# Kernel optimization log

Measured on AMD Instinct MI355X. Metric: run time of the kernel, lower is better.

Reference implementation:

```python
import jax, jax.numpy as jnp
import numpy as np

# ---- fixed config (Linear_mvm defaults, XBAR 64x64) ----
ROW = 64; COL = 64
BIT_SLICE = 2; BIT_STREAM = 1
W_BITS = 16; W_FRAC = 12          # weight_bit_frac = weight_bits//4*3
I_BITS = 16; I_FRAC = 12          # input_bit_frac  = input_bits//4*3
ADC_BIT = 8                       # log2(ROW) + bit_slice (bit_stream==1)
ACM_BITS = 16; ACM_FRAC = 12
BSN = W_BITS // BIT_SLICE         # 8 slices per weight, MSB-first columns
STN = I_BITS // BIT_STREAM        # 16 input bit-streams, LSB-first
IN_F = 1024; OUT_F = 1024; BATCH = 256


def _bit_slice_weight(w_nonneg):
    # w_nonneg: [out, in] nonnegative -> sliced crossbar matrix [in, out*BSN] (MSB->LSB per channel)
    w_int = jnp.clip(jnp.round(w_nonneg * (2.0 ** W_FRAC)), 0.0, 2.0 ** W_BITS - 1.0)
    shifts = (BIT_SLICE * (BSN - 1 - jnp.arange(BSN))).astype(jnp.float32)
    sl = jnp.floor(w_int[..., None] / (2.0 ** shifts)) % (2 ** BIT_SLICE)  # [out,in,BSN]
    o, i = w_nonneg.shape
    return sl.transpose(1, 0, 2).reshape(i, o * BSN)


def _input_bits(x):
    # two's-complement fixed point, LSB-first bit planes: [b, in, STN]
    x_int = jnp.clip(jnp.round(x * (2.0 ** I_FRAC)), -(2.0 ** (I_BITS - 1)), 2.0 ** (I_BITS - 1) - 1.0)
    x_u = jnp.where(x_int < 0, x_int + 2.0 ** I_BITS, x_int)
    return jnp.floor(x_u[..., None] / (2.0 ** jnp.arange(I_BITS, dtype=jnp.float32))) % 2.0


def _tile(mat, r, c):
    # pad to tile multiples and reshape to [xr, xc, r, c]
    pr = (-mat.shape[0]) % r; pc = (-mat.shape[1]) % c
    m = jnp.pad(mat, ((0, pr), (0, pc)))
    xr, xc = m.shape[0] // r, m.shape[1] // c
    return m.reshape(xr, r, xc, c).transpose(0, 2, 1, 3)


def _adc(a):
    # uniform ADC quantization of the analog column current to ADC_BIT bits
    full = float(ROW * (2 ** BIT_SLICE - 1))
    step = full / (2.0 ** ADC_BIT - 1.0)
    return jnp.clip(jnp.round(a / step) * step, 0.0, full)


def _mvm_one_sign(bits_tiled, xbars):
    # bits_tiled [b, xr, ROW, STN]; xbars [xr, xc, ROW, COL]
    sw_slice = 2.0 ** (BIT_SLICE * (BSN - 1 - jnp.arange(BSN, dtype=jnp.float32)))  # MSB..LSB
    sw_stream = 2.0 ** (BIT_STREAM * jnp.arange(STN, dtype=jnp.float32))
    sw_stream = sw_stream.at[-1].multiply(-1.0)  # two's-complement MSB stream

    def step(acc, si):
        bi, w = si                                   # bi [b,xr,ROW]
        analog = jnp.einsum('brk,rckj->brcj', bi, xbars)  # [b,xr,xc,COL]
        analog = _adc(analog)
        b, xr, xc, _ = analog.shape
        dig = analog.reshape(b, xr, xc, COL // BSN, BSN) @ sw_slice  # shift-add slices
        return acc + w * dig, None

    b = bits_tiled.shape[0]; xr, xc = xbars.shape[0], xbars.shape[1]
    acc0 = jnp.zeros((b, xr, xc, COL // BSN), jnp.float32)
    streams = jnp.moveaxis(bits_tiled, -1, 0)  # [STN, b, xr, ROW]
    acc, _ = jax.lax.scan(step, acc0, (streams, sw_stream))
    return acc.sum(axis=1).reshape(b, xc * (COL // BSN))  # sum row tiles, flatten channels


def _forward(x, weight, bias):
    pos = _bit_slice_weight(jnp.maximum(weight, 0.0))
    neg = _bit_slice_weight(-jnp.minimum(weight, 0.0))
    xb_pos = _tile(pos, ROW, COL)
    xb_neg = _tile(neg, ROW, COL)
    bits = _input_bits(x)                                  # [b,in,STN]
    xr = xb_pos.shape[0]
    bits = jnp.pad(bits, ((0, 0), (0, xr * ROW - bits.shape[1]), (0, 0)))
    bits = bits.reshape(x.shape[0], xr, ROW, STN)
    out = _mvm_one_sign(bits, xb_pos) - _mvm_one_sign(bits, xb_neg)
    out = out * (2.0 ** (-(W_FRAC + I_FRAC)))              # undo fixed-point scaling
    # accumulator quantization to ACM_BITS / ACM_FRAC
    out = jnp.clip(jnp.round(out * 2.0 ** ACM_FRAC), -(2.0 ** (ACM_BITS - 1)), 2.0 ** (ACM_BITS - 1) - 1.0) * 2.0 ** (-ACM_FRAC)
    out = out[:, :OUT_F]
    return out + bias[None, :]


def setup_inputs() -> dict:
    key = jax.random.key(0)
    k1, k2, k3 = jax.random.split(key, 3)
    x = jax.random.normal(k1, (BATCH, IN_F), jnp.float32)
    weight = jax.random.normal(k2, (OUT_F, IN_F), jnp.float32) * 0.05  # representable in Q4.12
    bias = jax.random.normal(k3, (OUT_F,), jnp.float32) * 0.05
    return {"x": x, "weight": weight, "bias": bias}


def reference(x, weight, bias):
    return _forward(x, weight, bias)
```

## Files before the change

kernel.cpp:

```cpp
#include <hip/hip_runtime.h>
#include <stdint.h>

#define BATCH 256
#define IN_F  1024
#define OUT_F 1024
#define RT    16
#define STN   16
#define NCOL  16384

typedef int   v4i  __attribute__((ext_vector_type(4)));
typedef int   v16i __attribute__((ext_vector_type(16)));
typedef float v2f  __attribute__((ext_vector_type(2)));

#define AP_SZ ((size_t)STN * BATCH * IN_F)
#define BP_SZ ((size_t)64 * NCOL * 16)

__global__ __launch_bounds__(256) void pack_fused(
    const float* __restrict__ x, const float* __restrict__ w,
    uint8_t* __restrict__ Ap2, uint8_t* __restrict__ Bp,
    uint32_t* __restrict__ flags)
{
    if (blockIdx.x < 512) {
        int item = blockIdx.x * 256 + threadIdx.x;
        int o  = item & 1023;
        int sg = (item >> 10) & 1;
        int g  = item >> 11;
        const float* wr = w + (size_t)o * IN_F + g * 16;
        uint32_t wq[16];
        #pragma unroll
        for (int j = 0; j < 16; ++j) {
            float wv = wr[j];
            float wf = rintf(fmaxf(sg ? -wv : wv, 0.0f) * 4096.0f);
            wq[j] = (uint32_t)fminf(wf, 65535.0f);
        }
        uint32_t nzmask = 0;
        #pragma unroll
        for (int s = 0; s < 8; ++s) {
            int sh = 14 - 2 * s;
            uint32_t dw[4], nz = 0;
            #pragma unroll
            for (int q = 0; q < 4; ++q) {
                uint32_t d = 0;
                #pragma unroll
                for (int j = 0; j < 4; ++j)
                    d |= ((wq[q * 4 + j] >> sh) & 3u) << (8 * j);
                dw[q] = d;
                nz |= d;
            }
            int sgs = sg * 8 + s;
            *(uint4*)(Bp + (size_t)(g * NCOL + sgs * 1024 + o) * 16) =
                make_uint4(dw[0], dw[1], dw[2], dw[3]);
            nzmask |= (nz ? 1u : 0u) << s;
        }
        int r = g >> 2, ob = o >> 7;
        #pragma unroll
        for (int s = 0; s < 8; ++s) {
            int any = __any((int)((nzmask >> s) & 1u));
            if (any && (threadIdx.x & 63) == 0)
                atomicOr(&flags[(sg * 8 + s) * 8 + ob], 1u << r);
        }
    } else {
        int item = (blockIdx.x - 512) * 256 + threadIdx.x;
        int b  = item & 255;
        int tq = (item >> 8) & 3;
        int kg = item >> 10;
        int r = kg >> 2, f = (kg >> 1) & 1, hi = kg & 1;
        int y = b >> 5, l = hi * 32 + (b & 31);
        const float* xr = x + (size_t)b * IN_F + kg * 16;
        uint32_t xu[16];
        #pragma unroll
        for (int j = 0; j < 16; ++j) {
            float xf = rintf(xr[j] * 4096.0f);
            xf = fminf(fmaxf(xf, -32768.0f), 32767.0f);
            xu[j] = (uint32_t)((int)xf) & 0xFFFFu;
        }
        uint8_t* wbase = Ap2 + ((size_t)(r * 8 + y) * 16) * 2048 + f * 1024 + l * 16;
        #pragma unroll
        for (int tt = 0; tt < 4; ++tt) {
            int t = tq * 4 + tt;
            uint32_t dw[4];
            #pragma unroll
            for (int q = 0; q < 4; ++q) {
                uint32_t d = 0;
                #pragma unroll
                for (int j = 0; j < 4; ++j)
                    d |= ((xu[q * 4 + j] >> t) & 1u) << (8 * j);
                dw[q] = d;
            }
            *(uint4*)(wbase + t * 2048) = make_uint4(dw[0], dw[1], dw[2], dw[3]);
        }
    }
}

__global__ __launch_bounds__(256, 4) void cim_mfma(
    const uint8_t* __restrict__ Ap2, const uint8_t* __restrict__ Bp,
    const uint32_t* __restrict__ flags, float* __restrict__ out)
{
    const float MAG = 12582912.0f;
    int tid = threadIdx.x, wid = tid >> 6, l = tid & 63, h2 = l >> 5;

    uint32_t f0 = flags[l], f1 = flags[64 + l];
    int pc0 = __popc(f0), pc1 = __popc(f1);
    int total = __popcll(__ballot(pc0 > 0)) + __popcll(__ballot(pc1 > 0));
    int idx = blockIdx.x >> 2, z = blockIdx.x & 3;
    if (idx >= total) return;
    unsigned long long lt = (1ULL << l) - 1;
    int rank0 = 0, rank1 = 0;
    #pragma unroll
    for (int v = 16; v >= 1; --v) {
        unsigned long long m0 = __ballot(pc0 == v);
        unsigned long long m1 = __ballot(pc1 == v);
        int c = __popcll(m0) + __popcll(m1);
        rank0 += (pc0 < v) ? c : ((pc0 == v) ? __popcll(m0 & lt) : 0);
        rank1 += (pc1 < v) ? c : ((pc1 == v) ? (__popcll(m0) + __popcll(m1 & lt)) : 0);
    }
    unsigned long long s0 = __ballot(rank0 == idx);
    unsigned long long s1 = __ballot(rank1 == idx);
    int p = s0 ? __builtin_ctzll(s0) : (64 + __builtin_ctzll(s1));
    int sgs = p >> 3, ob = p & 7;
    uint32_t fb = flags[p];

    int y = blockIdx.y;
    int s = sgs & 7, sg = sgs >> 3;
    int col = sgs * 1024 + ob * 128 + wid * 32 + (l & 31);
    float clane = ldexpf(192.0f / 255.0f, 14 - 2 * s);
    if (sg) clane = -clane;

    v2f acc2[8];
    #pragma unroll
    for (int i = 0; i < 8; ++i) acc2[i] = (v2f)0.0f;
    v16i zero;
    #pragma unroll
    for (int i = 0; i < 16; ++i) zero[i] = 0;

    int rank = 0, nproc = 0;
    for (int r = 0; r < RT; ++r) {
        if (!((fb >> r) & 1u)) continue;
        if ((rank++ & 3) != z) continue;
        ++nproc;

        v4i bf0 = *(const v4i*)(Bp + ((size_t)(r * 4 + h2)     * NCOL + col) * 16);
        v4i bf1 = *(const v4i*)(Bp + ((size_t)(r * 4 + 2 + h2) * NCOL + col) * 16);

        const uint8_t* abase = Ap2 + ((size_t)(r * 8 + y) * 16) * 2048 + l * 16;
        #pragma unroll 4
        for (int t = 0; t < STN; ++t) {
            const uint8_t* ap = abase + t * 2048;
            v4i af0 = *(const v4i*)ap;
            v4i af1 = *(const v4i*)(ap + 1024);
            v16i c = __builtin_amdgcn_mfma_i32_32x32x32_i8(af0, bf0, zero, 0, 0, 0);
            c      = __builtin_amdgcn_mfma_i32_32x32x32_i8(af1, bf1, c,    0, 0, 0);
            float wt = (t == 15) ? -32768.0f : (float)(1 << t);
            float cw = clane * wt;
            #pragma unroll
            for (int i = 0; i < 8; ++i) {
                v2f af; af.x = (float)c[2 * i]; af.y = (float)c[2 * i + 1];
                v2f tq;
                tq.x = fmaf(af.x, 1.328125f, MAG);
                tq.y = fmaf(af.y, 1.328125f, MAG);
                v2f qf = tq - MAG;
                acc2[i].x = fmaf(qf.x, cw, acc2[i].x);
                acc2[i].y = fmaf(qf.y, cw, acc2[i].y);
            }
        }
    }

    if (nproc == 0) return;
    int o = ob * 128 + wid * 32 + (l & 31);
    #pragma unroll
    for (int i = 0; i < 16; ++i) {
        int b = y * 32 + (i & 3) + 8 * (i >> 2) + 4 * h2;
        float v = (i & 1) ? acc2[i >> 1].y : acc2[i >> 1].x;
        atomicAdd(&out[(size_t)b * OUT_F + o], v);
    }
}

__global__ __launch_bounds__(256) void finalize(
    float* __restrict__ out, const float* __restrict__ bias)
{
    int idx = blockIdx.x * 256 + threadIdx.x;
    int o = idx & (OUT_F - 1);
    float ov = out[idx] * 0x1p-24f;
    float q = rintf(ov * 4096.0f);
    q = fminf(fmaxf(q, -32768.0f), 32767.0f);
    out[idx] = q * 0x1p-12f + bias[o];
}

extern "C" void kernel_launch(void* const* d_in, const int* in_sizes, int n_in,
                              void* d_out, int out_size, void* d_ws, size_t ws_size,
                              hipStream_t stream) {
    const float* x    = (const float*)d_in[0];
    const float* w    = (const float*)d_in[1];
    const float* bias = (const float*)d_in[2];
    float* out = (float*)d_out;

    uint8_t*  Ap2   = (uint8_t*)d_ws;
    uint8_t*  Bp    = Ap2 + AP_SZ;
    uint32_t* flags = (uint32_t*)(Bp + BP_SZ);

    hipMemsetAsync(flags, 0, 128 * sizeof(uint32_t), stream);
    hipMemsetAsync(out, 0, (size_t)BATCH * OUT_F * sizeof(float), stream);
    hipLaunchKernelGGL(pack_fused, dim3(768), dim3(256), 0, stream,
                       x, w, Ap2, Bp, flags);
    hipLaunchKernelGGL(cim_mfma, dim3(512, 8), dim3(256), 0, stream,
                       Ap2, Bp, flags, out);
    hipLaunchKernelGGL(finalize, dim3(BATCH * OUT_F / 256), dim3(256), 0, stream,
                       out, bias);
}
```

Measured before the change: 180.1 us.

## Replace atomic split-K MFMA kernel with per-block LDS reduction and fused finalize

The work split changes. Each block now owns a 32-column output slice for one batch tile, and its 8 waves share the flagged (slice,row-tile) pairs round-robin. Partial sums are reduced in LDS, then quantized with bias added inside the same kernel. This removes the global atomicAdds, the output memset and the separate finalize launch. In exchange the grid drops to 256 blocks of 512 threads, which may cut occupancy, and waves can end up with unbalanced work.

```diff
diff --git a/kernel.cpp b/kernel.cpp
--- a/kernel.cpp
+++ b/kernel.cpp
@@ -92,39 +92,18 @@
     }
 }
 
-__global__ __launch_bounds__(256, 4) void cim_mfma(
+__global__ __launch_bounds__(512) void cim_block(
     const uint8_t* __restrict__ Ap2, const uint8_t* __restrict__ Bp,
-    const uint32_t* __restrict__ flags, float* __restrict__ out)
+    const uint32_t* __restrict__ flags, const float* __restrict__ bias,
+    float* __restrict__ out)
 {
+    __shared__ float red[8 * 1024];
     const float MAG = 12582912.0f;
     int tid = threadIdx.x, wid = tid >> 6, l = tid & 63, h2 = l >> 5;
+    int oq = blockIdx.x, y = blockIdx.y;
+    int ob = oq >> 2;
 
-    uint32_t f0 = flags[l], f1 = flags[64 + l];
-    int pc0 = __popc(f0), pc1 = __popc(f1);
-    int total = __popcll(__ballot(pc0 > 0)) + __popcll(__ballot(pc1 > 0));
-    int idx = blockIdx.x >> 2, z = blockIdx.x & 3;
-    if (idx >= total) return;
-    unsigned long long lt = (1ULL << l) - 1;
-    int rank0 = 0, rank1 = 0;
-    #pragma unroll
-    for (int v = 16; v >= 1; --v) {
-        unsigned long long m0 = __ballot(pc0 == v);
-        unsigned long long m1 = __ballot(pc1 == v);
-        int c = __popcll(m0) + __popcll(m1);
-        rank0 += (pc0 < v) ? c : ((pc0 == v) ? __popcll(m0 & lt) : 0);
-        rank1 += (pc1 < v) ? c : ((pc1 == v) ? (__popcll(m0) + __popcll(m1 & lt)) : 0);
-    }
-    unsigned long long s0 = __ballot(rank0 == idx);
-    unsigned long long s1 = __ballot(rank1 == idx);
-    int p = s0 ? __builtin_ctzll(s0) : (64 + __builtin_ctzll(s1));
-    int sgs = p >> 3, ob = p & 7;
-    uint32_t fb = flags[p];
-
-    int y = blockIdx.y;
-    int s = sgs & 7, sg = sgs >> 3;
-    int col = sgs * 1024 + ob * 128 + wid * 32 + (l & 31);
-    float clane = ldexpf(192.0f / 255.0f, 14 - 2 * s);
-    if (sg) clane = -clane;
+    uint32_t fw = flags[(l & 15) * 8 + ob];
 
     v2f acc2[8];
     #pragma unroll
@@ -133,57 +112,67 @@
     #pragma unroll
     for (int i = 0; i < 16; ++i) zero[i] = 0;
 
-    int rank = 0, nproc = 0;
+    int cnt = 0;
     for (int r = 0; r < RT; ++r) {
-        if (!((fb >> r) & 1u)) continue;
-        if ((rank++ & 3) != z) continue;
-        ++nproc;
+        uint32_t smask = (uint32_t)(__ballot((int)((fw >> r) & 1u))) & 0xFFFFu;
+        while (smask) {
+            int sgs = __builtin_ctz(smask);
+            smask &= smask - 1;
+            if ((cnt++ & 7) != wid) continue;
 
-        v4i bf0 = *(const v4i*)(Bp + ((size_t)(r * 4 + h2)     * NCOL + col) * 16);
-        v4i bf1 = *(const v4i*)(Bp + ((size_t)(r * 4 + 2 + h2) * NCOL + col) * 16);
+            int s = sgs & 7, sg = sgs >> 3;
+            float clane = __int_as_float((141 - 2 * s) << 23) * (192.0f / 255.0f);
+            if (sg) clane = -clane;
+            int col = sgs * 1024 + oq * 32 + (l & 31);
 
-        const uint8_t* abase = Ap2 + ((size_t)(r * 8 + y) * 16) * 2048 + l * 16;
-        #pragma unroll 4
-        for (int t = 0; t < STN; ++t) {
-            const uint8_t* ap = abase + t * 2048;
-            v4i af0 = *(const v4i*)ap;
-            v4i af1 = *(const v4i*)(ap + 1024);
-            v16i c = __builtin_amdgcn_mfma_i32_32x32x32_i8(af0, bf0, zero, 0, 0, 0);
-            c      = __builtin_amdgcn_mfma_i32_32x32x32_i8(af1, bf1, c,    0, 0, 0);
-            float wt = (t == 15) ? -32768.0f : (float)(1 << t);
-            float cw = clane * wt;
-            #pragma unroll
-            for (int i = 0; i < 8; ++i) {
-                v2f af; af.x = (float)c[2 * i]; af.y = (float)c[2 * i + 1];
-                v2f tq;
-                tq.x = fmaf(af.x, 1.328125f, MAG);
-                tq.y = fmaf(af.y, 1.328125f, MAG);
-                v2f qf = tq - MAG;
-                acc2[i].x = fmaf(qf.x, cw, acc2[i].x);
-                acc2[i].y = fmaf(qf.y, cw, acc2[i].y);
+            v4i bf0 = *(const v4i*)(Bp + ((size_t)(r * 4 + h2)     * NCOL + col) * 16);
+            v4i bf1 = *(const v4i*)(Bp + ((size_t)(r * 4 + 2 + h2) * NCOL + col) * 16);
+
+            const uint8_t* abase = Ap2 + ((size_t)(r * 8 + y) * 16) * 2048 + l * 16;
+            #pragma unroll 4
+            for (int t = 0; t < STN; ++t) {
+                const uint8_t* ap = abase + t * 2048;
+                v4i af0 = *(const v4i*)ap;
+                v4i af1 = *(const v4i*)(ap + 1024);
+                v16i c = __builtin_amdgcn_mfma_i32_32x32x32_i8(af0, bf0, zero, 0, 0, 0);
+                c      = __builtin_amdgcn_mfma_i32_32x32x32_i8(af1, bf1, c,    0, 0, 0);
+                float wt = (t == 15) ? -32768.0f : (float)(1 << t);
+                float cw = clane * wt;
+                #pragma unroll
+                for (int i = 0; i < 8; ++i) {
+                    v2f af; af.x = (float)c[2 * i]; af.y = (float)c[2 * i + 1];
+                    v2f tq;
+                    tq.x = fmaf(af.x, 1.328125f, MAG);
+                    tq.y = fmaf(af.y, 1.328125f, MAG);
+                    v2f qf = tq - MAG;
+                    acc2[i].x = fmaf(qf.x, cw, acc2[i].x);
+                    acc2[i].y = fmaf(qf.y, cw, acc2[i].y);
+                }
             }
         }
     }
 
-    if (nproc == 0) return;
-    int o = ob * 128 + wid * 32 + (l & 31);
+    float* slot = red + wid * 1024 + l * 16;
     #pragma unroll
-    for (int i = 0; i < 16; ++i) {
-        int b = y * 32 + (i & 3) + 8 * (i >> 2) + 4 * h2;
-        float v = (i & 1) ? acc2[i >> 1].y : acc2[i >> 1].x;
-        atomicAdd(&out[(size_t)b * OUT_F + o], v);
+    for (int i = 0; i < 8; ++i) {
+        slot[2 * i]     = acc2[i].x;
+        slot[2 * i + 1] = acc2[i].y;
     }
-}
-
-__global__ __launch_bounds__(256) void finalize(
-    float* __restrict__ out, const float* __restrict__ bias)
-{
-    int idx = blockIdx.x * 256 + threadIdx.x;
-    int o = idx & (OUT_F - 1);
-    float ov = out[idx] * 0x1p-24f;
-    float q = rintf(ov * 4096.0f);
-    q = fminf(fmaxf(q, -32768.0f), 32767.0f);
-    out[idx] = q * 0x1p-12f + bias[o];
+    __syncthreads();
+    #pragma unroll
+    for (int k = 0; k < 2; ++k) {
+        int e = k * 512 + tid;
+        float v = 0.0f;
+        #pragma unroll
+        for (int w = 0; w < 8; ++w) v += red[w * 1024 + e];
+        int ll = e >> 4, i = e & 15;
+        int b = y * 32 + (i & 3) + 8 * (i >> 2) + 4 * (ll >> 5);
+        int o = oq * 32 + (ll & 31);
+        float ov = v * 0x1p-24f;
+        float q = rintf(ov * 4096.0f);
+        q = fminf(fmaxf(q, -32768.0f), 32767.0f);
+        out[(size_t)b * OUT_F + o] = q * 0x1p-12f + bias[o];
+    }
 }
 
 extern "C" void kernel_launch(void* const* d_in, const int* in_sizes, int n_in,
@@ -199,11 +188,8 @@
     uint32_t* flags = (uint32_t*)(Bp + BP_SZ);
 
     hipMemsetAsync(flags, 0, 128 * sizeof(uint32_t), stream);
-    hipMemsetAsync(out, 0, (size_t)BATCH * OUT_F * sizeof(float), stream);
     hipLaunchKernelGGL(pack_fused, dim3(768), dim3(256), 0, stream,
                        x, w, Ap2, Bp, flags);
-    hipLaunchKernelGGL(cim_mfma, dim3(512, 8), dim3(256), 0, stream,
-                       Ap2, Bp, flags, out);
-    hipLaunchKernelGGL(finalize, dim3(BATCH * OUT_F / 256), dim3(256), 0, stream,
-                       out, bias);
+    hipLaunchKernelGGL(cim_block, dim3(32, 8), dim3(512), 0, stream,
+                       Ap2, Bp, flags, bias, out);
 }
```

Result: faster. 175.3 us (-2.7%).
